# Kernel optimization log

Measured on AMD Instinct MI355X. Metric: run time of the kernel, lower is better.

## Reference

```python
import jax, jax.numpy as jnp
import numpy as np

N, E, DIN, DH, H, L = 8192, 32768, 1024, 256, 8, 3
NEG_SLOPE = 0.2  # PyG GATv2Conv default


def setup_inputs() -> dict:
    key = jax.random.key(0)
    ks = jax.random.split(key, 16)
    s = 0.05
    p = {}
    p["x"] = jax.random.normal(ks[0], (N, DIN), jnp.float32)
    p["edge_index"] = jax.random.randint(ks[1], (2, E), 0, N, jnp.int32)
    p["edge_attr"] = jax.random.randint(ks[2], (E,), 0, 5, jnp.int32)
    p["node_types"] = jax.random.randint(ks[3], (N,), 0, 5, jnp.int32)
    # input_proj (input_dim != hidden_dim so it is a Linear)
    p["W_in"] = jax.random.normal(ks[4], (DIN, DH), jnp.float32) * s
    p["b_in"] = jnp.zeros((DH,), jnp.float32)
    p["node_emb"] = jax.random.normal(ks[5], (5, DH), jnp.float32) * s
    p["edge_emb"] = jax.random.normal(ks[6], (5, DH), jnp.float32) * s
    # per-layer GATv2 params, stacked over L layers
    p["Wl"] = jax.random.normal(ks[7], (L, DH, H * DH), jnp.float32) * s   # lin_l
    p["bl"] = jnp.zeros((L, H * DH), jnp.float32)
    p["Wr"] = jax.random.normal(ks[8], (L, DH, H * DH), jnp.float32) * s   # lin_r
    p["br"] = jnp.zeros((L, H * DH), jnp.float32)
    p["We"] = jax.random.normal(ks[9], (L, DH, H * DH), jnp.float32) * s   # lin_edge (no bias)
    p["att"] = jax.random.normal(ks[10], (L, H, DH), jnp.float32) * s
    p["b_gat"] = jnp.zeros((L, DH), jnp.float32)                            # out bias (concat=False)
    p["W_out"] = jax.random.normal(ks[11], (DH, DH), jnp.float32) * s
    p["b_out"] = jnp.zeros((DH,), jnp.float32)
    return p


def _gatv2(h, src, dst, ea, Wl, bl, Wr, br, We, att, bias):
    n = h.shape[0]
    # add self loops; edge_attr fill_value='mean' = segment-mean of incoming edge attrs
    loop = jnp.arange(n, dtype=src.dtype)
    cnt = jax.ops.segment_sum(jnp.ones(dst.shape, jnp.float32), dst, num_segments=n)
    loop_ea = jax.ops.segment_sum(ea, dst, num_segments=n) / jnp.maximum(cnt, 1.0)[:, None]
    src2 = jnp.concatenate([src, loop])
    dst2 = jnp.concatenate([dst, loop])
    ea2 = jnp.concatenate([ea, loop_ea], axis=0)
    xl = (h @ Wl + bl).reshape(n, H, DH)   # source transform
    xr = (h @ Wr + br).reshape(n, H, DH)   # target transform
    ee = (ea2 @ We).reshape(-1, H, DH)     # edge transform [E2,H,C]
    z = jax.nn.leaky_relu(xl[src2] + xr[dst2] + ee, NEG_SLOPE)   # [E2,H,C]
    logits = jnp.einsum('ehc,hc->eh', z, att)                    # [E2,H]
    # numerically stable segment softmax over edges sharing a target node
    lmax = jax.ops.segment_max(logits, dst2, num_segments=n)     # [N,H]
    pnum = jnp.exp(logits - lmax[dst2])
    alpha = pnum / jax.ops.segment_sum(pnum, dst2, num_segments=n)[dst2]
    out = jax.ops.segment_sum(alpha[:, :, None] * xl[src2], dst2, num_segments=n)  # [N,H,C]
    return out.mean(axis=1) + bias          # concat=False -> head mean + bias


def reference(x, edge_index, edge_attr, node_types, W_in, b_in, node_emb, edge_emb,
              Wl, bl, Wr, br, We, att, b_gat, W_out, b_out):
    src, dst = edge_index[0], edge_index[1]
    h = x @ W_in + b_in + node_emb[node_types]
    for l in range(L):
        ea = edge_emb[edge_attr]
        h = jax.nn.relu(_gatv2(h, src, dst, ea, Wl[l], bl[l], Wr[l], br[l], We[l], att[l], b_gat[l]))
        # dropout p=0.1 is a no-op in eval mode
    return h @ W_out + b_out
```

## Files before the change

### kernel.cpp

```cpp
#include <hip/hip_runtime.h>

#define N_NODES 8192
#define N_EDGES 32768
#define D_IN    1024
#define DH      256
#define NH      8
#define HD      2048
#define NL      3
#define NT      5
#define NEG     0.2f
#define PADK    40

typedef __bf16 bf16x8 __attribute__((ext_vector_type(8)));
typedef float  f32x4  __attribute__((ext_vector_type(4)));
typedef unsigned short ushort8 __attribute__((ext_vector_type(8)));

static __device__ __forceinline__ unsigned short f2bf(float f) {
    unsigned u = __float_as_uint(f);
    unsigned r = (u + 0x7FFFu + ((u >> 16) & 1u)) >> 16;
    return (unsigned short)r;
}
static __device__ __forceinline__ float bf2f(unsigned short h) {
    return __uint_as_float(((unsigned)h) << 16);
}

__global__ __launch_bounds__(256) void split_act(
    const float* __restrict__ X, unsigned short* __restrict__ A3,
    int MK, int kshift)
{
    int idx = blockIdx.x * 256 + threadIdx.x;
    if (idx >= MK) return;
    int K = 1 << kshift;
    int m = idx >> kshift, k = idx & (K - 1);
    float v = X[idx];
    unsigned short hu = f2bf(v);
    unsigned short lu = f2bf(v - bf2f(hu));
    size_t b = (size_t)m * 3 * K + k;
    A3[b]         = hu;
    A3[b + K]     = hu;
    A3[b + 2 * K] = lu;
}

__global__ __launch_bounds__(256) void split_w(
    const float* __restrict__ W, unsigned short* __restrict__ B3T,
    int K, int N)
{
    __shared__ float t[32][33];
    int k0 = blockIdx.y * 32, n0 = blockIdx.x * 32;
    int tid = threadIdx.x;
    int r = tid >> 5, c = tid & 31;
    for (int rr = r; rr < 32; rr += 8)
        t[rr][c] = W[(size_t)(k0 + rr) * N + n0 + c];
    __syncthreads();
    for (int rr = r; rr < 32; rr += 8) {
        int n = n0 + rr, k = k0 + c;
        float v = t[c][rr];
        unsigned short hu = f2bf(v);
        unsigned short lu = f2bf(v - bf2f(hu));
        size_t b = (size_t)n * 3 * K + k;
        B3T[b]         = hu;
        B3T[b + K]     = lu;
        B3T[b + 2 * K] = hu;
    }
}

__global__ __launch_bounds__(256) void gemm_mfma(
    const unsigned short* __restrict__ A3, const unsigned short* __restrict__ B3T,
    const float* __restrict__ bias, float* __restrict__ C,
    int M, int N, int K3,
    const float* __restrict__ emb, const int* __restrict__ types)
{
    __shared__ unsigned short aLds[128 * PADK];
    __shared__ unsigned short bLds[128 * PADK];
    const int tid = threadIdx.x;
    const int m0 = blockIdx.y * 128, n0 = blockIdx.x * 128;
    const int lane = tid & 63, wid = tid >> 6;
    const int wm = wid >> 1, wn = wid & 1;
    const int srow = tid >> 2, scq = (tid & 3) * 8;
    const int frow = lane & 15, fkq = (lane >> 4) * 8;

    f32x4 acc[4][4] = {};

    for (int kt = 0; kt < K3; kt += 32) {
#pragma unroll
        for (int rnd = 0; rnd < 2; rnd++) {
            int row = rnd * 64 + srow;
            ushort8 av = *(const ushort8*)(A3 + (size_t)(m0 + row) * K3 + kt + scq);
            ushort8 bv = *(const ushort8*)(B3T + (size_t)(n0 + row) * K3 + kt + scq);
            *(ushort8*)(aLds + row * PADK + scq) = av;
            *(ushort8*)(bLds + row * PADK + scq) = bv;
        }
        __syncthreads();
        bf16x8 af[4], bf[4];
#pragma unroll
        for (int f = 0; f < 4; f++) {
            af[f] = *(const bf16x8*)(aLds + (wm * 64 + f * 16 + frow) * PADK + fkq);
            bf[f] = *(const bf16x8*)(bLds + (wn * 64 + f * 16 + frow) * PADK + fkq);
        }
#pragma unroll
        for (int i = 0; i < 4; i++)
#pragma unroll
            for (int j = 0; j < 4; j++)
                acc[i][j] = __builtin_amdgcn_mfma_f32_16x16x32_bf16(
                    af[i], bf[j], acc[i][j], 0, 0, 0);
        __syncthreads();
    }

    const int ccol = lane & 15, crq = (lane >> 4) * 4;
#pragma unroll
    for (int j = 0; j < 4; j++) {
        int gcol = n0 + wn * 64 + j * 16 + ccol;
        float bv = bias[gcol];
#pragma unroll
        for (int i = 0; i < 4; i++) {
#pragma unroll
            for (int r = 0; r < 4; r++) {
                int grow = m0 + wm * 64 + i * 16 + crq + r;
                float v = acc[i][j][r] + bv;
                if (emb) v += emb[types[grow] * DH + gcol];
                C[(size_t)grow * N + gcol] = v;
            }
        }
    }
}

__global__ __launch_bounds__(256) void e5_kernel(
    const float* __restrict__ eemb, const float* __restrict__ We,
    float* __restrict__ E5)
{
    int col = blockIdx.x * 256 + threadIdx.x;
    int t = blockIdx.y;
    float acc = 0.f;
    for (int k = 0; k < DH; k++) acc += eemb[t * DH + k] * We[(size_t)k * HD + col];
    E5[(size_t)t * HD + col] = acc;
}

__global__ void deg_hist(const int* __restrict__ dst, const int* __restrict__ attr,
                         int* cnt, int* hist)
{
    int e = blockIdx.x * 256 + threadIdx.x;
    if (e < N_EDGES) {
        int d = dst[e];
        atomicAdd(&cnt[d], 1);
        atomicAdd(&hist[d * NT + attr[e]], 1);
    }
}

__global__ __launch_bounds__(256) void scan_kernel(const int* __restrict__ cnt,
                                                   int* __restrict__ rowptr)
{
    __shared__ int part[256];
    int tid = threadIdx.x;
    int base = tid * 32, s = 0;
    for (int i = 0; i < 32; i++) s += cnt[base + i];
    part[tid] = s;
    __syncthreads();
    for (int off = 1; off < 256; off <<= 1) {
        int v = (tid >= off) ? part[tid - off] : 0;
        __syncthreads();
        part[tid] += v;
        __syncthreads();
    }
    int run = (tid == 0) ? 0 : part[tid - 1];
    for (int i = 0; i < 32; i++) { rowptr[base + i] = run; run += cnt[base + i]; }
    if (tid == 255) rowptr[N_NODES] = run;
}

__global__ void csr_fill(const int* __restrict__ dst, const int* __restrict__ rowptr,
                         int* fillc, int* __restrict__ csr)
{
    int e = blockIdx.x * 256 + threadIdx.x;
    if (e < N_EDGES) {
        int d = dst[e];
        int p = atomicAdd(&fillc[d], 1);
        csr[rowptr[d] + p] = e;
    }
}

__global__ __launch_bounds__(256) void gat_online(
    const float* __restrict__ xl, const float* __restrict__ xr,
    const float* __restrict__ E5, const float* __restrict__ att,
    const int* __restrict__ csr, const int* __restrict__ rowptr,
    const int* __restrict__ cnt, const int* __restrict__ src,
    const int* __restrict__ attr, const int* __restrict__ hist,
    const float* __restrict__ bgat, float* __restrict__ hout)
{
    const int n = blockIdx.x, tid = threadIdx.x;
    const int h = tid >> 5, cb = tid & 31;
    const int base = h * DH + cb * 8;
    __shared__ float outs[NH][DH];

    const int deg = cnt[n];
    const int r0 = rowptr[n];

    float4 xr0 = *(const float4*)(xr + (size_t)n * HD + base);
    float4 xr1 = *(const float4*)(xr + (size_t)n * HD + base + 4);
    float4 at0 = *(const float4*)(att + base);
    float4 at1 = *(const float4*)(att + base + 4);

    float m = -1e30f, d = 0.f;
    float O0 = 0.f, O1 = 0.f, O2 = 0.f, O3 = 0.f;
    float O4 = 0.f, O5 = 0.f, O6 = 0.f, O7 = 0.f;

    for (int i = 0; i <= deg; i++) {
        const bool isloop = (i == deg);
        int s, a = 0;
        if (isloop) { s = n; }
        else { int e = csr[r0 + i]; s = src[e]; a = attr[e]; }

        const float* xp = xl + (size_t)s * HD + base;
        float4 v0 = *(const float4*)xp;
        float4 v1 = *(const float4*)(xp + 4);

        float4 e0, e1;
        if (isloop) {
            float inv = 1.f / fmaxf((float)deg, 1.f);
            e0 = make_float4(0.f, 0.f, 0.f, 0.f);
            e1 = make_float4(0.f, 0.f, 0.f, 0.f);
#pragma unroll
            for (int t = 0; t < NT; t++) {
                float wt = inv * (float)hist[n * NT + t];
                float4 q0 = *(const float4*)(E5 + (size_t)t * HD + base);
                float4 q1 = *(const float4*)(E5 + (size_t)t * HD + base + 4);
                e0.x += wt * q0.x; e0.y += wt * q0.y; e0.z += wt * q0.z; e0.w += wt * q0.w;
                e1.x += wt * q1.x; e1.y += wt * q1.y; e1.z += wt * q1.z; e1.w += wt * q1.w;
            }
        } else {
            e0 = *(const float4*)(E5 + (size_t)a * HD + base);
            e1 = *(const float4*)(E5 + (size_t)a * HD + base + 4);
        }

        float z, lsum = 0.f;
        z = v0.x + xr0.x + e0.x; z = (z >= 0.f) ? z : NEG * z; lsum += z * at0.x;
        z = v0.y + xr0.y + e0.y; z = (z >= 0.f) ? z : NEG * z; lsum += z * at0.y;
        z = v0.z + xr0.z + e0.z; z = (z >= 0.f) ? z : NEG * z; lsum += z * at0.z;
        z = v0.w + xr0.w + e0.w; z = (z >= 0.f) ? z : NEG * z; lsum += z * at0.w;
        z = v1.x + xr1.x + e1.x; z = (z >= 0.f) ? z : NEG * z; lsum += z * at1.x;
        z = v1.y + xr1.y + e1.y; z = (z >= 0.f) ? z : NEG * z; lsum += z * at1.y;
        z = v1.z + xr1.z + e1.z; z = (z >= 0.f) ? z : NEG * z; lsum += z * at1.z;
        z = v1.w + xr1.w + e1.w; z = (z >= 0.f) ? z : NEG * z; lsum += z * at1.w;

#pragma unroll
        for (int off = 16; off; off >>= 1) lsum += __shfl_xor(lsum, off, 32);

        float nm = fmaxf(m, lsum);
        float scale = __expf(m - nm);
        float p = __expf(lsum - nm);
        O0 = O0 * scale + p * v0.x; O1 = O1 * scale + p * v0.y;
        O2 = O2 * scale + p * v0.z; O3 = O3 * scale + p * v0.w;
        O4 = O4 * scale + p * v1.x; O5 = O5 * scale + p * v1.y;
        O6 = O6 * scale + p * v1.z; O7 = O7 * scale + p * v1.w;
        d = d * scale + p;
        m = nm;
    }

    float invd = 1.f / d;
    float4 w0 = make_float4(O0 * invd, O1 * invd, O2 * invd, O3 * invd);
    float4 w1 = make_float4(O4 * invd, O5 * invd, O6 * invd, O7 * invd);
    *(float4*)(&outs[h][cb * 8])     = w0;
    *(float4*)(&outs[h][cb * 8 + 4]) = w1;
    __syncthreads();

    float o = 0.f;
#pragma unroll
    for (int hh = 0; hh < NH; hh++) o += outs[hh][tid];
    o = o * 0.125f + bgat[tid];
    hout[(size_t)n * DH + tid] = fmaxf(o, 0.f);
}

extern "C" void kernel_launch(void* const* d_in, const int* in_sizes, int n_in,
                              void* d_out, int out_size, void* d_ws, size_t ws_size,
                              hipStream_t stream)
{
    const float* x     = (const float*)d_in[0];
    const int*   eidx  = (const int*)d_in[1];
    const int*   src   = eidx;
    const int*   dst   = eidx + N_EDGES;
    const int*   attr  = (const int*)d_in[2];
    const int*   types = (const int*)d_in[3];
    const float* W_in  = (const float*)d_in[4];
    const float* b_in  = (const float*)d_in[5];
    const float* nemb  = (const float*)d_in[6];
    const float* eemb  = (const float*)d_in[7];
    const float* Wl    = (const float*)d_in[8];
    const float* bl    = (const float*)d_in[9];
    const float* Wr    = (const float*)d_in[10];
    const float* br    = (const float*)d_in[11];
    const float* We    = (const float*)d_in[12];
    const float* att   = (const float*)d_in[13];
    const float* bgat  = (const float*)d_in[14];
    const float* W_out = (const float*)d_in[15];
    const float* b_out = (const float*)d_in[16];
    float* out = (float*)d_out;

    char* ws = (char*)d_ws;
    size_t off = 0;
    auto alloc = [&](size_t bytes) -> void* {
        void* p = ws + off;
        off += (bytes + 255) & ~(size_t)255;
        return p;
    };
    float* h      = (float*)alloc((size_t)N_NODES * DH * 4);
    float* xl     = (float*)alloc((size_t)N_NODES * HD * 4);
    float* xr     = (float*)alloc((size_t)N_NODES * HD * 4);
    float* E5     = (float*)alloc((size_t)NT * HD * 4);
    int* cnt      = (int*)alloc((size_t)N_NODES * 4);
    int* hist     = (int*)alloc((size_t)N_NODES * NT * 4);
    int* rowptr   = (int*)alloc((size_t)(N_NODES + 1) * 4);
    int* fillc    = (int*)alloc((size_t)N_NODES * 4);
    int* csr      = (int*)alloc((size_t)N_EDGES * 4);
    unsigned short* A3  = (unsigned short*)alloc((size_t)N_NODES * 3 * D_IN * 2);
    unsigned short* B3T = (unsigned short*)alloc((size_t)HD * 3 * D_IN * 2);

    hipMemsetAsync(cnt, 0, (size_t)N_NODES * 4, stream);
    hipMemsetAsync(hist, 0, (size_t)N_NODES * NT * 4, stream);
    hipMemsetAsync(fillc, 0, (size_t)N_NODES * 4, stream);

    deg_hist<<<(N_EDGES + 255) / 256, 256, 0, stream>>>(dst, attr, cnt, hist);
    scan_kernel<<<1, 256, 0, stream>>>(cnt, rowptr);
    csr_fill<<<(N_EDGES + 255) / 256, 256, 0, stream>>>(dst, rowptr, fillc, csr);

    split_act<<<(N_NODES * D_IN) / 256, 256, 0, stream>>>(x, A3, N_NODES * D_IN, 10);
    split_w<<<dim3(DH / 32, D_IN / 32), 256, 0, stream>>>(W_in, B3T, D_IN, DH);
    gemm_mfma<<<dim3(DH / 128, N_NODES / 128), 256, 0, stream>>>(
        A3, B3T, b_in, h, N_NODES, DH, 3 * D_IN, nemb, types);

    for (int l = 0; l < NL; l++) {
        const float* Wl_l = Wl + (size_t)l * DH * HD;
        const float* Wr_l = Wr + (size_t)l * DH * HD;
        const float* We_l = We + (size_t)l * DH * HD;

        split_act<<<(N_NODES * DH) / 256, 256, 0, stream>>>(h, A3, N_NODES * DH, 8);
        split_w<<<dim3(HD / 32, DH / 32), 256, 0, stream>>>(Wl_l, B3T, DH, HD);
        gemm_mfma<<<dim3(HD / 128, N_NODES / 128), 256, 0, stream>>>(
            A3, B3T, bl + (size_t)l * HD, xl, N_NODES, HD, 3 * DH, nullptr, nullptr);
        split_w<<<dim3(HD / 32, DH / 32), 256, 0, stream>>>(Wr_l, B3T, DH, HD);
        gemm_mfma<<<dim3(HD / 128, N_NODES / 128), 256, 0, stream>>>(
            A3, B3T, br + (size_t)l * HD, xr, N_NODES, HD, 3 * DH, nullptr, nullptr);

        e5_kernel<<<dim3(HD / 256, NT), 256, 0, stream>>>(eemb, We_l, E5);
        gat_online<<<N_NODES, 256, 0, stream>>>(
            xl, xr, E5, att + (size_t)l * NH * DH, csr, rowptr, cnt, src, attr,
            hist, bgat + (size_t)l * DH, h);
    }

    split_act<<<(N_NODES * DH) / 256, 256, 0, stream>>>(h, A3, N_NODES * DH, 8);
    split_w<<<dim3(DH / 32, DH / 32), 256, 0, stream>>>(W_out, B3T, DH, DH);
    gemm_mfma<<<dim3(DH / 128, N_NODES / 128), 256, 0, stream>>>(
        A3, B3T, b_out, out, N_NODES, DH, 3 * DH, nullptr, nullptr);
}
```

Before: 895.9 us.

## Rework bf16x3 GEMM with direct global-to-LDS loads, swizzle, BK64, split-K

```diff
diff --git a/kernel.cpp b/kernel.cpp
--- a/kernel.cpp
+++ b/kernel.cpp
@@ -9,7 +9,6 @@
 #define NL      3
 #define NT      5
 #define NEG     0.2f
-#define PADK    40
 
 typedef __bf16 bf16x8 __attribute__((ext_vector_type(8)));
 typedef float  f32x4  __attribute__((ext_vector_type(4)));
@@ -23,22 +22,36 @@
 static __device__ __forceinline__ float bf2f(unsigned short h) {
     return __uint_as_float(((unsigned)h) << 16);
 }
-
-__global__ __launch_bounds__(256) void split_act(
+static __device__ __forceinline__ void gload_lds16(const void* g, void* l) {
+    __builtin_amdgcn_global_load_lds(
+        (const __attribute__((address_space(1))) unsigned*)g,
+        (__attribute__((address_space(3))) unsigned*)l, 16, 0, 0);
+}
+
+__global__ __launch_bounds__(256) void split_act8(
     const float* __restrict__ X, unsigned short* __restrict__ A3,
-    int MK, int kshift)
+    int MK8, int k8shift)
 {
     int idx = blockIdx.x * 256 + threadIdx.x;
-    if (idx >= MK) return;
-    int K = 1 << kshift;
-    int m = idx >> kshift, k = idx & (K - 1);
-    float v = X[idx];
-    unsigned short hu = f2bf(v);
-    unsigned short lu = f2bf(v - bf2f(hu));
-    size_t b = (size_t)m * 3 * K + k;
-    A3[b]         = hu;
-    A3[b + K]     = hu;
-    A3[b + 2 * K] = lu;
+    if (idx >= MK8) return;
+    int K8 = 1 << k8shift;
+    int K = K8 << 3;
+    int m = idx >> k8shift, k8 = idx & (K8 - 1);
+    const float* xp = X + (size_t)m * K + k8 * 8;
+    float4 v0 = *(const float4*)xp;
+    float4 v1 = *(const float4*)(xp + 4);
+    float vv[8] = {v0.x, v0.y, v0.z, v0.w, v1.x, v1.y, v1.z, v1.w};
+    ushort8 hi, lo;
+#pragma unroll
+    for (int j = 0; j < 8; j++) {
+        unsigned short h = f2bf(vv[j]);
+        hi[j] = h;
+        lo[j] = f2bf(vv[j] - bf2f(h));
+    }
+    size_t b = (size_t)m * 3 * K + k8 * 8;
+    *(ushort8*)(A3 + b)         = hi;
+    *(ushort8*)(A3 + b + K)     = hi;
+    *(ushort8*)(A3 + b + 2 * K) = lo;
 }
 
 __global__ __launch_bounds__(256) void split_w(
@@ -64,62 +77,94 @@
     }
 }
 
+__global__ __launch_bounds__(256) void init_c(
+    float* __restrict__ C, const float* __restrict__ bias, int MN, int nshift,
+    const float* __restrict__ emb, const int* __restrict__ types)
+{
+    for (int idx = blockIdx.x * 256 + threadIdx.x; idx < MN; idx += gridDim.x * 256) {
+        int col = idx & ((1 << nshift) - 1);
+        float v = bias[col];
+        if (emb) v += emb[types[idx >> nshift] * DH + col];
+        C[idx] = v;
+    }
+}
+
 __global__ __launch_bounds__(256) void gemm_mfma(
     const unsigned short* __restrict__ A3, const unsigned short* __restrict__ B3T,
     const float* __restrict__ bias, float* __restrict__ C,
-    int M, int N, int K3,
-    const float* __restrict__ emb, const int* __restrict__ types)
-{
-    __shared__ unsigned short aLds[128 * PADK];
-    __shared__ unsigned short bLds[128 * PADK];
+    int M, int N, int K3, int kslice)
+{
+    __shared__ unsigned short aLds[128 * 64];
+    __shared__ unsigned short bLds[128 * 64];
     const int tid = threadIdx.x;
     const int m0 = blockIdx.y * 128, n0 = blockIdx.x * 128;
-    const int lane = tid & 63, wid = tid >> 6;
-    const int wm = wid >> 1, wn = wid & 1;
-    const int srow = tid >> 2, scq = (tid & 3) * 8;
-    const int frow = lane & 15, fkq = (lane >> 4) * 8;
+    const int lane = tid & 63, w = tid >> 6;
+    const int wm = w >> 1, wn = w & 1;
+    const int srow8 = lane >> 3;
+    const int schunk = lane & 7;
+    const int frow = lane & 15, fchunk = lane >> 4;
+    const int kt0 = blockIdx.z * kslice;
+    const int kt1 = kt0 + kslice;
 
     f32x4 acc[4][4] = {};
 
-    for (int kt = 0; kt < K3; kt += 32) {
-#pragma unroll
-        for (int rnd = 0; rnd < 2; rnd++) {
-            int row = rnd * 64 + srow;
-            ushort8 av = *(const ushort8*)(A3 + (size_t)(m0 + row) * K3 + kt + scq);
-            ushort8 bv = *(const ushort8*)(B3T + (size_t)(n0 + row) * K3 + kt + scq);
-            *(ushort8*)(aLds + row * PADK + scq) = av;
-            *(ushort8*)(bLds + row * PADK + scq) = bv;
+    for (int kt = kt0; kt < kt1; kt += 64) {
+#pragma unroll
+        for (int q = 0; q < 4; q++) {
+            int row = (q * 4 + w) * 8 + srow8;
+            int scol = (schunk << 4) ^ ((row & 7) << 4);
+            char* ldst_a = (char*)aLds + (q * 4 + w) * 1024;
+            char* ldst_b = (char*)bLds + (q * 4 + w) * 1024;
+            gload_lds16(A3 + (size_t)(m0 + row) * K3 + kt + (scol >> 1), ldst_a);
+            gload_lds16(B3T + (size_t)(n0 + row) * K3 + kt + (scol >> 1), ldst_b);
         }
         __syncthreads();
-        bf16x8 af[4], bf[4];
-#pragma unroll
-        for (int f = 0; f < 4; f++) {
-            af[f] = *(const bf16x8*)(aLds + (wm * 64 + f * 16 + frow) * PADK + fkq);
-            bf[f] = *(const bf16x8*)(bLds + (wn * 64 + f * 16 + frow) * PADK + fkq);
+#pragma unroll
+        for (int kh = 0; kh < 2; kh++) {
+            const int c = kh * 4 + fchunk;
+            bf16x8 af[4], bfr[4];
+#pragma unroll
+            for (int f = 0; f < 4; f++) {
+                int ra = wm * 64 + f * 16 + frow;
+                af[f] = *(const bf16x8*)((const char*)aLds + ra * 128 + ((c ^ (ra & 7)) << 4));
+                int rb = wn * 64 + f * 16 + frow;
+                bfr[f] = *(const bf16x8*)((const char*)bLds + rb * 128 + ((c ^ (rb & 7)) << 4));
+            }
+#pragma unroll
+            for (int i = 0; i < 4; i++)
+#pragma unroll
+                for (int j = 0; j < 4; j++)
+                    acc[i][j] = __builtin_amdgcn_mfma_f32_16x16x32_bf16(
+                        af[i], bfr[j], acc[i][j], 0, 0, 0);
         }
-#pragma unroll
-        for (int i = 0; i < 4; i++)
-#pragma unroll
-            for (int j = 0; j < 4; j++)
-                acc[i][j] = __builtin_amdgcn_mfma_f32_16x16x32_bf16(
-                    af[i], bf[j], acc[i][j], 0, 0, 0);
         __syncthreads();
     }
 
     const int ccol = lane & 15, crq = (lane >> 4) * 4;
-#pragma unroll
-    for (int j = 0; j < 4; j++) {
-        int gcol = n0 + wn * 64 + j * 16 + ccol;
-        float bv = bias[gcol];
-#pragma unroll
-        for (int i = 0; i < 4; i++) {
-#pragma unroll
-            for (int r = 0; r < 4; r++) {
-                int grow = m0 + wm * 64 + i * 16 + crq + r;
-                float v = acc[i][j][r] + bv;
-                if (emb) v += emb[types[grow] * DH + gcol];
-                C[(size_t)grow * N + gcol] = v;
-            }
+    if (gridDim.z == 1) {
+#pragma unroll
+        for (int j = 0; j < 4; j++) {
+            int gcol = n0 + wn * 64 + j * 16 + ccol;
+            float bv = bias[gcol];
+#pragma unroll
+            for (int i = 0; i < 4; i++)
+#pragma unroll
+                for (int r = 0; r < 4; r++) {
+                    int grow = m0 + wm * 64 + i * 16 + crq + r;
+                    C[(size_t)grow * N + gcol] = acc[i][j][r] + bv;
+                }
+        }
+    } else {
+#pragma unroll
+        for (int j = 0; j < 4; j++) {
+            int gcol = n0 + wn * 64 + j * 16 + ccol;
+#pragma unroll
+            for (int i = 0; i < 4; i++)
+#pragma unroll
+                for (int r = 0; r < 4; r++) {
+                    int grow = m0 + wm * 64 + i * 16 + crq + r;
+                    atomicAdd(&C[(size_t)grow * N + gcol], acc[i][j][r]);
+                }
         }
     }
 }
@@ -320,23 +365,26 @@
     scan_kernel<<<1, 256, 0, stream>>>(cnt, rowptr);
     csr_fill<<<(N_EDGES + 255) / 256, 256, 0, stream>>>(dst, rowptr, fillc, csr);
 
-    split_act<<<(N_NODES * D_IN) / 256, 256, 0, stream>>>(x, A3, N_NODES * D_IN, 10);
+    split_act8<<<(N_NODES * D_IN / 8 + 255) / 256, 256, 0, stream>>>(
+        x, A3, N_NODES * D_IN / 8, 7);
     split_w<<<dim3(DH / 32, D_IN / 32), 256, 0, stream>>>(W_in, B3T, D_IN, DH);
-    gemm_mfma<<<dim3(DH / 128, N_NODES / 128), 256, 0, stream>>>(
-        A3, B3T, b_in, h, N_NODES, DH, 3 * D_IN, nemb, types);
+    init_c<<<2048, 256, 0, stream>>>(h, b_in, N_NODES * DH, 8, nemb, types);
+    gemm_mfma<<<dim3(DH / 128, N_NODES / 128, 8), 256, 0, stream>>>(
+        A3, B3T, nullptr, h, N_NODES, DH, 3 * D_IN, 3 * D_IN / 8);
 
     for (int l = 0; l < NL; l++) {
         const float* Wl_l = Wl + (size_t)l * DH * HD;
         const float* Wr_l = Wr + (size_t)l * DH * HD;
         const float* We_l = We + (size_t)l * DH * HD;
 
-        split_act<<<(N_NODES * DH) / 256, 256, 0, stream>>>(h, A3, N_NODES * DH, 8);
+        split_act8<<<(N_NODES * DH / 8 + 255) / 256, 256, 0, stream>>>(
+            h, A3, N_NODES * DH / 8, 5);
         split_w<<<dim3(HD / 32, DH / 32), 256, 0, stream>>>(Wl_l, B3T, DH, HD);
-        gemm_mfma<<<dim3(HD / 128, N_NODES / 128), 256, 0, stream>>>(
-            A3, B3T, bl + (size_t)l * HD, xl, N_NODES, HD, 3 * DH, nullptr, nullptr);
+        gemm_mfma<<<dim3(HD / 128, N_NODES / 128, 1), 256, 0, stream>>>(
+            A3, B3T, bl + (size_t)l * HD, xl, N_NODES, HD, 3 * DH, 3 * DH);
         split_w<<<dim3(HD / 32, DH / 32), 256, 0, stream>>>(Wr_l, B3T, DH, HD);
-        gemm_mfma<<<dim3(HD / 128, N_NODES / 128), 256, 0, stream>>>(
-            A3, B3T, br + (size_t)l * HD, xr, N_NODES, HD, 3 * DH, nullptr, nullptr);
+        gemm_mfma<<<dim3(HD / 128, N_NODES / 128, 1), 256, 0, stream>>>(
+            A3, B3T, br + (size_t)l * HD, xr, N_NODES, HD, 3 * DH, 3 * DH);
 
         e5_kernel<<<dim3(HD / 256, NT), 256, 0, stream>>>(eemb, We_l, E5);
         gat_online<<<N_NODES, 256, 0, stream>>>(
@@ -344,8 +392,10 @@
             hist, bgat + (size_t)l * DH, h);
     }
 
-    split_act<<<(N_NODES * DH) / 256, 256, 0, stream>>>(h, A3, N_NODES * DH, 8);
+    split_act8<<<(N_NODES * DH / 8 + 255) / 256, 256, 0, stream>>>(
+        h, A3, N_NODES * DH / 8, 5);
     split_w<<<dim3(DH / 32, DH / 32), 256, 0, stream>>>(W_out, B3T, DH, DH);
-    gemm_mfma<<<dim3(DH / 128, N_NODES / 128), 256, 0, stream>>>(
-        A3, B3T, b_out, out, N_NODES, DH, 3 * DH, nullptr, nullptr);
-}
+    init_c<<<2048, 256, 0, stream>>>(out, b_out, N_NODES * DH, 8, nullptr, nullptr);
+    gemm_mfma<<<dim3(DH / 128, N_NODES / 128, 4), 256, 0, stream>>>(
+        A3, B3T, nullptr, out, N_NODES, DH, 3 * DH, 3 * DH / 4);
+}
```

New measurement: 805.0 us. -10.2%, faster.
